# Kernel tuning notes

Measured on AMD Instinct MI355X. Metric: run time of the kernel, lower is better.

Reference implementation:

```python
import jax, jax.numpy as jnp
import numpy as np

D_IN, N_HEADS, N_KV, HEAD_DIM = 2048, 8, 4, 256
GROUP = N_HEADS // N_KV
SCALING = 256.0 ** -0.5  # query_pre_attn_scalar = 256
EPS = 1e-6


def _rms_norm(x, gamma):
    # Gemma-style RMSNorm with (1 + gamma) scale, over last dim (head_dim)
    var = jnp.mean(x * x, axis=-1, keepdims=True)
    return x * jax.lax.rsqrt(var + EPS) * (1.0 + gamma)


def _apply_rope(x, cos, sin):
    # x: [b, h, s, d]; cos/sin: [s, d] (rotate-half convention)
    d = x.shape[-1]
    x1, x2 = x[..., : d // 2], x[..., d // 2:]
    rotated = jnp.concatenate([-x2, x1], axis=-1)
    return x * cos[None, None] + rotated * sin[None, None]


def setup_inputs() -> dict:
    key = jax.random.key(0)
    ks = jax.random.split(key, 6)
    b, s = 2, 2048
    x = jax.random.normal(ks[0], (b, s, D_IN), dtype=jnp.float32)
    # causal mask: True above diagonal = masked
    mask = jnp.triu(jnp.ones((s, s), dtype=bool), k=1)
    # RoPE tables (base 10000)
    inv_freq = 1.0 / (10000.0 ** (jnp.arange(0, HEAD_DIM, 2, dtype=jnp.float32) / HEAD_DIM))
    angles = jnp.arange(s, dtype=jnp.float32)[:, None] * inv_freq[None, :]  # [s, d/2]
    angles = jnp.concatenate([angles, angles], axis=-1)  # [s, d]
    cos, sin = jnp.cos(angles), jnp.sin(angles)
    std = 0.02
    wq = jax.random.normal(ks[1], (N_HEADS * HEAD_DIM, D_IN), dtype=jnp.float32) * std
    wk = jax.random.normal(ks[2], (N_KV * HEAD_DIM, D_IN), dtype=jnp.float32) * std
    wv = jax.random.normal(ks[3], (N_KV * HEAD_DIM, D_IN), dtype=jnp.float32) * std
    wo = jax.random.normal(ks[4], (D_IN, N_HEADS * HEAD_DIM), dtype=jnp.float32) * std
    q_gamma = jnp.zeros((HEAD_DIM,), dtype=jnp.float32)
    k_gamma = jnp.zeros((HEAD_DIM,), dtype=jnp.float32)
    return {"x": x, "mask": mask, "cos": cos, "sin": sin,
            "wq": wq, "wk": wk, "wv": wv, "wo": wo,
            "q_gamma": q_gamma, "k_gamma": k_gamma}


def reference(x, mask, cos, sin, wq, wk, wv, wo, q_gamma, k_gamma):
    b, s, _ = x.shape
    # projections (torch Linear: y = x @ W.T)
    q = (x @ wq.T).reshape(b, s, N_HEADS, HEAD_DIM).transpose(0, 2, 1, 3)  # [b,H,s,d]
    k = (x @ wk.T).reshape(b, s, N_KV, HEAD_DIM).transpose(0, 2, 1, 3)     # [b,G,s,d]
    v = (x @ wv.T).reshape(b, s, N_KV, HEAD_DIM).transpose(0, 2, 1, 3)     # [b,G,s,d]
    q = _rms_norm(q, q_gamma)
    k = _rms_norm(k, k_gamma)
    q = _apply_rope(q, cos, sin) * SCALING
    k = _apply_rope(k, cos, sin)
    # GQA via broadcast (avoids repeat_interleave): head h = g*GROUP + j (group-major)
    qg = q.reshape(b, N_KV, GROUP, s, HEAD_DIM)
    scores = jnp.einsum('bgjqd,bgkd->bgjqk', qg, k)  # [b,G,group,s,s]
    scores = jnp.where(mask[None, None, None], -jnp.inf, scores)
    weights = jax.nn.softmax(scores, axis=-1)
    ctx = jnp.einsum('bgjqk,bgkd->bgjqd', weights, v)  # [b,G,group,s,d]
    ctx = ctx.reshape(b, N_HEADS, s, HEAD_DIM).transpose(0, 2, 1, 3).reshape(b, s, N_HEADS * HEAD_DIM)
    return ctx @ wo.T
```

## Files before the change

kernel.cpp:

```cpp
#include <hip/hip_runtime.h>
#include <math.h>


typedef __bf16 bf16x8 __attribute__((ext_vector_type(8)));
typedef __bf16 bf16x4 __attribute__((ext_vector_type(4)));
typedef float  f32x4  __attribute__((ext_vector_type(4)));

#define MFMA16(a, b, c) __builtin_amdgcn_mfma_f32_16x16x32_bf16(a, b, c, 0, 0, 0)

__device__ __forceinline__ void async16(const __bf16* g, const __bf16* l) {
  __builtin_amdgcn_global_load_lds(
      (__attribute__((address_space(1))) const void*)g,
      (__attribute__((address_space(3))) void*)l, 16, 0, 0);
}

__global__ __launch_bounds__(256) void cast_f32_bf16(
    const float* __restrict__ src, __bf16* __restrict__ dst) {
  const size_t i = ((size_t)blockIdx.x * 256 + threadIdx.x) * 4;
  f32x4 v = *(const f32x4*)(src + i);
  bf16x4 o;
#pragma unroll
  for (int j = 0; j < 4; j++) o[j] = (__bf16)v[j];
  *(bf16x4*)(dst + i) = o;
}

template <typename OT>
__device__ __forceinline__ void gemm_body(const __bf16* A, const __bf16* B,
                                          OT* C, size_t m0, size_t n0,
                                          size_t ccol0, int ldc) {
  constexpr int K = 2048;
  __shared__ __align__(16) __bf16 As[128 * 32];
  __shared__ __align__(16) __bf16 Bs[128 * 32];
  const int tid = threadIdx.x;
  const int wave = tid >> 6, lane = tid & 63;
  const int lr = lane & 15, lq = lane >> 4;
  const int wm = (wave >> 1) * 64, wn = (wave & 1) * 64;

  f32x4 acc[4][4];
#pragma unroll
  for (int i = 0; i < 4; i++)
#pragma unroll
    for (int j = 0; j < 4; j++)
#pragma unroll
      for (int r = 0; r < 4; r++) acc[i][j][r] = 0.f;

  int srow[2], skof[2];
#pragma unroll
  for (int c = 0; c < 2; c++) {
    const int t = wave * 2 + c;
    const int g = t * 8 + (lane >> 3);
    const int cc = (lane & 7) ^ (g & 7);
    srow[c] = g * 2 + (cc >> 2);
    skof[c] = (cc & 3) * 8;
  }

  for (int k0 = 0; k0 < K; k0 += 32) {
#pragma unroll
    for (int c = 0; c < 2; c++) {
      const int t = wave * 2 + c;
      async16(A + (m0 + srow[c]) * K + k0 + skof[c], As + t * 512);
      async16(B + (n0 + srow[c]) * K + k0 + skof[c], Bs + t * 512);
    }
    __syncthreads();
    bf16x8 af[4], bf[4];
#pragma unroll
    for (int i = 0; i < 4; i++) {
      const int row = wm + i * 16 + lr;
      const int g = row >> 1;
      const int p = ((row & 1) * 4 + lq) ^ (g & 7);
      af[i] = *(const bf16x8*)&As[g * 64 + p * 8];
    }
#pragma unroll
    for (int j = 0; j < 4; j++) {
      const int row = wn + j * 16 + lr;
      const int g = row >> 1;
      const int p = ((row & 1) * 4 + lq) ^ (g & 7);
      bf[j] = *(const bf16x8*)&Bs[g * 64 + p * 8];
    }
#pragma unroll
    for (int i = 0; i < 4; i++)
#pragma unroll
      for (int j = 0; j < 4; j++)
        acc[i][j] = MFMA16(af[i], bf[j], acc[i][j]);
    __syncthreads();
  }

#pragma unroll
  for (int i = 0; i < 4; i++)
#pragma unroll
    for (int j = 0; j < 4; j++)
#pragma unroll
      for (int r = 0; r < 4; r++) {
        const size_t row = m0 + wm + i * 16 + lq * 4 + r;
        const size_t col = ccol0 + wn + j * 16 + lr;
        C[row * (size_t)ldc + col] = (OT)acc[i][j][r];
      }
}

template <typename OT>
__global__ __launch_bounds__(256) void gemm_bt(
    const __bf16* __restrict__ A, const __bf16* __restrict__ B,
    OT* __restrict__ C, const int ldc) {
  gemm_body<OT>(A, B, C, (size_t)blockIdx.y * 128, (size_t)blockIdx.x * 128,
                (size_t)blockIdx.x * 128, ldc);
}

__global__ __launch_bounds__(256) void gemm_qkv(
    const __bf16* __restrict__ A, const __bf16* __restrict__ Bq,
    const __bf16* __restrict__ Bk, const __bf16* __restrict__ Bv,
    __bf16* __restrict__ C) {
  const int bx = blockIdx.x;
  const __bf16* B;
  int nl;
  if (bx < 16) { B = Bq; nl = bx; }
  else if (bx < 24) { B = Bk; nl = bx - 16; }
  else { B = Bv; nl = bx - 24; }
  gemm_body<__bf16>(A, B, C, (size_t)blockIdx.y * 128, (size_t)nl * 128,
                    (size_t)bx * 128, 4096);
}

__global__ __launch_bounds__(256) void rmsrope(
    const __bf16* __restrict__ qkv, const float* __restrict__ cosb,
    const float* __restrict__ sinb, const float* __restrict__ qg,
    const float* __restrict__ kg, __bf16* __restrict__ qrot,
    __bf16* __restrict__ krot) {
  const int wave = threadIdx.x >> 6, lane = threadIdx.x & 63;
  const int rid = blockIdx.x * 4 + wave;
  const int m = rid / 12, seg = rid % 12;
  const int b = m >> 11, pos = m & 2047;
  const bool isq = seg < 8;
  const int col = isq ? seg * 256 : 2048 + (seg - 8) * 256;
  const int d = lane * 4;

  bf16x4 xv = *(const bf16x4*)(qkv + (size_t)m * 4096 + col + d);
  float x[4];
#pragma unroll
  for (int i = 0; i < 4; i++) x[i] = (float)xv[i];
  float ss = x[0] * x[0] + x[1] * x[1] + x[2] * x[2] + x[3] * x[3];
#pragma unroll
  for (int off = 1; off < 64; off <<= 1) ss += __shfl_xor(ss, off);
  const float inv = rsqrtf(ss * (1.f / 256.f) + 1e-6f);

  f32x4 gv = *(const f32x4*)((isq ? qg : kg) + d);
  float xn[4];
#pragma unroll
  for (int i = 0; i < 4; i++) xn[i] = x[i] * inv * (1.f + gv[i]);
  float rot[4];
#pragma unroll
  for (int i = 0; i < 4; i++) {
    const float pn = __shfl_xor(xn[i], 32);
    rot[i] = (lane < 32) ? -pn : pn;
  }
  f32x4 cv = *(const f32x4*)(cosb + (size_t)pos * 256 + d);
  f32x4 sv = *(const f32x4*)(sinb + (size_t)pos * 256 + d);
  const float sc = isq ? 0.0625f : 1.f;
  bf16x4 ov;
#pragma unroll
  for (int i = 0; i < 4; i++)
    ov[i] = (__bf16)((xn[i] * cv[i] + rot[i] * sv[i]) * sc);
  __bf16* dst = isq
      ? qrot + ((size_t)(b * 8 + seg) * 2048 + pos) * 256 + d
      : krot + ((size_t)(b * 4 + (seg - 8)) * 2048 + pos) * 256 + d;
  *(bf16x4*)dst = ov;
}

__global__ __launch_bounds__(256) void vtrans(const __bf16* __restrict__ qkv,
                                              __bf16* __restrict__ vT) {
  __shared__ __bf16 tile[64 * 65];
  const int bkv = blockIdx.z;
  const int d0 = blockIdx.y * 64, p0 = blockIdx.x * 64;
  const int t = threadIdx.x;
  const int b = bkv >> 2, kv = bkv & 3;
#pragma unroll
  for (int i = 0; i < 16; i++) {
    const int f = i * 256 + t;
    const int pl = f >> 6, dl = f & 63;
    tile[pl * 65 + dl] =
        qkv[(size_t)(b * 2048 + p0 + pl) * 4096 + 3072 + kv * 256 + d0 + dl];
  }
  __syncthreads();
#pragma unroll
  for (int i = 0; i < 16; i++) {
    const int f = i * 256 + t;
    const int dl = f >> 6, pl = f & 63;
    vT[((size_t)bkv * 256 + d0 + dl) * 2048 + p0 + pl] = tile[pl * 65 + dl];
  }
}

__global__ __launch_bounds__(256) void flash(
    const __bf16* __restrict__ qrot, const __bf16* __restrict__ krot,
    const __bf16* __restrict__ vT, __bf16* __restrict__ ctx) {
  __shared__ __align__(16) __bf16 Ks[2][64 * 256];
  __shared__ __align__(16) __bf16 Vs[2][256 * 64];
  __shared__ __align__(16) __bf16 Ps[4 * 32 * 64];
  const int tid = threadIdx.x, wave = tid >> 6, lane = tid & 63;
  const int lr = lane & 15, lq = lane >> 4;
  const int Q = blockIdx.x;
  const int h = blockIdx.y, b = blockIdx.z, kv = h >> 1;
  const int q0 = Q * 128 + wave * 32;

  bf16x8 qf[2][8];
  {
    const __bf16* qbb = qrot + (size_t)(b * 8 + h) * 2048 * 256;
#pragma unroll
    for (int qi = 0; qi < 2; qi++)
#pragma unroll
      for (int i = 0; i < 8; i++)
        qf[qi][i] = *(const bf16x8*)(qbb + (size_t)(q0 + qi * 16 + lr) * 256 +
                                     i * 32 + lq * 8);
  }
  f32x4 acc[2][16];
#pragma unroll
  for (int qi = 0; qi < 2; qi++)
#pragma unroll
    for (int j = 0; j < 16; j++)
#pragma unroll
      for (int r = 0; r < 4; r++) acc[qi][j][r] = 0.f;
  float lsum[2][4];
#pragma unroll
  for (int qi = 0; qi < 2; qi++)
#pragma unroll
    for (int r = 0; r < 4; r++) lsum[qi][r] = 0.f;

  const __bf16* kbase = krot + (size_t)(b * 4 + kv) * 2048 * 256;
  const __bf16* vbase = vT + (size_t)(b * 4 + kv) * 256 * 2048;

  int koff[8], voff[8];
#pragma unroll
  for (int c = 0; c < 8; c++) {
    const int t = wave * 8 + c;
    {
      const int row = t * 2 + (lane >> 5);
      const int ch = (lane & 31) ^ (row & 31);
      koff[c] = row * 256 + ch * 8;
    }
    {
      const int d = t * 8 + (lane >> 3);
      const int ch = (lane & 7) ^ (d & 7);
      voff[c] = d * 2048 + ch * 8;
    }
  }

  const int nt = 2 * Q + 2;

#define STAGE(kt_, buf_)                                                   \
  {                                                                        \
    const int k0_ = (kt_)*64;                                              \
    _Pragma("unroll") for (int c = 0; c < 8; c++) {                        \
      const int t = wave * 8 + c;                                          \
      async16(kbase + (size_t)k0_ * 256 + koff[c], Ks[buf_] + t * 512);    \
      async16(vbase + k0_ + voff[c], Vs[buf_] + t * 512);                  \
    }                                                                      \
  }

  STAGE(0, 0);

  for (int kt = 0; kt < nt; kt++) {
    const int cur = kt & 1;
    const int k0 = kt * 64;
    if (kt + 1 < nt) {
      STAGE(kt + 1, cur ^ 1);
      asm volatile("s_waitcnt vmcnt(16)" ::: "memory");
    } else {
      asm volatile("s_waitcnt vmcnt(0)" ::: "memory");
    }
    __builtin_amdgcn_s_barrier();

    f32x4 s[2][4];
#pragma unroll
    for (int qi = 0; qi < 2; qi++)
#pragma unroll
      for (int f = 0; f < 4; f++)
#pragma unroll
        for (int r = 0; r < 4; r++) s[qi][f][r] = 0.f;
#pragma unroll
    for (int i = 0; i < 8; i++) {
      bf16x8 kf[4];
#pragma unroll
      for (int f = 0; f < 4; f++) {
        const int row = f * 16 + lr;
        const int pch = (i * 4 + lq) ^ (row & 31);
        kf[f] = *(const bf16x8*)&Ks[cur][row * 256 + pch * 8];
      }
#pragma unroll
      for (int qi = 0; qi < 2; qi++)
#pragma unroll
        for (int f = 0; f < 4; f++)
          s[qi][f] = MFMA16(qf[qi][i], kf[f], s[qi][f]);
    }

    const bool diag = (k0 + 63 > q0);
#pragma unroll
    for (int qi = 0; qi < 2; qi++) {
      const int qa = q0 + qi * 16 + lq * 4;
#pragma unroll
      for (int f = 0; f < 4; f++) {
        const int ka = k0 + f * 16 + lr;
        const int row = qi * 16 + lq * 4;
        const int pchb = (f * 2 + (lr >> 3));
#pragma unroll
        for (int r = 0; r < 4; r++) {
          float p = __expf(s[qi][f][r] - 16.f);
          if (diag && ka > qa + r) p = 0.f;
          lsum[qi][r] += p;
          Ps[wave * 2048 + (row + r) * 64 + (pchb ^ ((row + r) & 7)) * 8 +
             (lr & 7)] = (__bf16)p;
        }
      }
    }
    asm volatile("s_waitcnt lgkmcnt(0)" ::: "memory");

#pragma unroll
    for (int m = 0; m < 2; m++) {
      bf16x8 pf[2];
#pragma unroll
      for (int qi = 0; qi < 2; qi++) {
        const int row = qi * 16 + lr;
        const int pch = (m * 4 + lq) ^ (row & 7);
        pf[qi] = *(const bf16x8*)&Ps[wave * 2048 + row * 64 + pch * 8];
      }
#pragma unroll
      for (int j = 0; j < 16; j++) {
        const int d = j * 16 + lr;
        const int pch = (m * 4 + lq) ^ (d & 7);
        bf16x8 vf = *(const bf16x8*)&Vs[cur][d * 64 + pch * 8];
#pragma unroll
        for (int qi = 0; qi < 2; qi++)
          acc[qi][j] = MFMA16(pf[qi], vf, acc[qi][j]);
      }
    }
    __builtin_amdgcn_s_barrier();
  }
#undef STAGE

  float inv[2][4];
#pragma unroll
  for (int qi = 0; qi < 2; qi++)
#pragma unroll
    for (int r = 0; r < 4; r++) {
      float l = lsum[qi][r];
#pragma unroll
      for (int off = 1; off < 16; off <<= 1) l += __shfl_xor(l, off);
      inv[qi][r] = 1.f / l;
    }
#pragma unroll
  for (int qi = 0; qi < 2; qi++)
#pragma unroll
    for (int j = 0; j < 16; j++)
#pragma unroll
      for (int r = 0; r < 4; r++) {
        const int row = q0 + qi * 16 + lq * 4 + r;
        ctx[((size_t)(b * 2048 + row) * 8 + h) * 256 + j * 16 + lr] =
            (__bf16)(acc[qi][j][r] * inv[qi][r]);
      }
}

extern "C" void kernel_launch(void* const* d_in, const int* in_sizes, int n_in,
                              void* d_out, int out_size, void* d_ws,
                              size_t ws_size, hipStream_t stream) {
  const float* x = (const float*)d_in[0];
  const float* cosb = (const float*)d_in[2];
  const float* sinb = (const float*)d_in[3];
  const float* wq = (const float*)d_in[4];
  const float* wk = (const float*)d_in[5];
  const float* wv = (const float*)d_in[6];
  const float* wo = (const float*)d_in[7];
  const float* qg = (const float*)d_in[8];
  const float* kg = (const float*)d_in[9];
  float* out = (float*)d_out;

  char* ws = (char*)d_ws;
  __bf16* xbf = (__bf16*)ws;
  __bf16* wqbf = (__bf16*)(ws + ((size_t)16 << 20));
  __bf16* wkbf = (__bf16*)(ws + ((size_t)24 << 20));
  __bf16* wvbf = (__bf16*)(ws + ((size_t)28 << 20));
  __bf16* qkv = (__bf16*)(ws + ((size_t)32 << 20));
  __bf16* qrot = (__bf16*)ws;
  __bf16* krot = (__bf16*)(ws + ((size_t)16 << 20));
  __bf16* vTp = (__bf16*)(ws + ((size_t)24 << 20));
  __bf16* wobf = (__bf16*)(ws + ((size_t)32 << 20));
  __bf16* ctx = (__bf16*)(ws + ((size_t)40 << 20));

  cast_f32_bf16<<<8192, 256, 0, stream>>>(x, xbf);
  cast_f32_bf16<<<4096, 256, 0, stream>>>(wq, wqbf);
  cast_f32_bf16<<<2048, 256, 0, stream>>>(wk, wkbf);
  cast_f32_bf16<<<2048, 256, 0, stream>>>(wv, wvbf);

  gemm_qkv<<<dim3(32, 32), 256, 0, stream>>>(xbf, wqbf, wkbf, wvbf, qkv);

  rmsrope<<<12288, 256, 0, stream>>>(qkv, cosb, sinb, qg, kg, qrot, krot);
  vtrans<<<dim3(32, 4, 8), 256, 0, stream>>>(qkv, vTp);

  cast_f32_bf16<<<4096, 256, 0, stream>>>(wo, wobf);
  flash<<<dim3(16, 8, 2), 256, 0, stream>>>(qrot, krot, vTp, ctx);

  gemm_bt<float><<<dim3(16, 32), 256, 0, stream>>>(ctx, wobf, out, 2048);
}
```

Baseline: 425.8 us.

## Stage K/V tiles through registers instead of async global-to-LDS loads

```diff
diff --git a/kernel.cpp b/kernel.cpp
--- a/kernel.cpp
+++ b/kernel.cpp
@@ -187,7 +187,7 @@
   }
 }
 
-__global__ __launch_bounds__(256) void flash(
+__global__ __launch_bounds__(256, 1) void flash(
     const __bf16* __restrict__ qrot, const __bf16* __restrict__ krot,
     const __bf16* __restrict__ vT, __bf16* __restrict__ ctx) {
   __shared__ __align__(16) __bf16 Ks[2][64 * 256];
@@ -243,28 +243,33 @@
 
   const int nt = 2 * Q + 2;
 
-#define STAGE(kt_, buf_)                                                   \
+  bf16x8 kreg[8], vreg[8];
+
+#define KVLOAD(kt_)                                                        \
   {                                                                        \
     const int k0_ = (kt_)*64;                                              \
     _Pragma("unroll") for (int c = 0; c < 8; c++) {                        \
+      kreg[c] = *(const bf16x8*)(kbase + (size_t)k0_ * 256 + koff[c]);     \
+      vreg[c] = *(const bf16x8*)(vbase + k0_ + voff[c]);                   \
+    }                                                                      \
+  }
+#define KVWRITE(buf_)                                                      \
+  {                                                                        \
+    _Pragma("unroll") for (int c = 0; c < 8; c++) {                        \
       const int t = wave * 8 + c;                                          \
-      async16(kbase + (size_t)k0_ * 256 + koff[c], Ks[buf_] + t * 512);    \
-      async16(vbase + k0_ + voff[c], Vs[buf_] + t * 512);                  \
+      *(bf16x8*)&Ks[buf_][t * 512 + lane * 8] = kreg[c];                   \
+      *(bf16x8*)&Vs[buf_][t * 512 + lane * 8] = vreg[c];                   \
     }                                                                      \
   }
 
-  STAGE(0, 0);
+  KVLOAD(0);
+  KVWRITE(0);
+  __syncthreads();
 
   for (int kt = 0; kt < nt; kt++) {
     const int cur = kt & 1;
     const int k0 = kt * 64;
-    if (kt + 1 < nt) {
-      STAGE(kt + 1, cur ^ 1);
-      asm volatile("s_waitcnt vmcnt(16)" ::: "memory");
-    } else {
-      asm volatile("s_waitcnt vmcnt(0)" ::: "memory");
-    }
-    __builtin_amdgcn_s_barrier();
+    if (kt + 1 < nt) KVLOAD(kt + 1);
 
     f32x4 s[2][4];
 #pragma unroll
@@ -329,9 +334,12 @@
           acc[qi][j] = MFMA16(pf[qi], vf, acc[qi][j]);
       }
     }
-    __builtin_amdgcn_s_barrier();
-  }
-#undef STAGE
+
+    if (kt + 1 < nt) KVWRITE(cur ^ 1);
+    __syncthreads();
+  }
+#undef KVLOAD
+#undef KVWRITE
 
   float inv[2][4];
 #pragma unroll
```

Measured after the change: 434.2 us. No clear change (+2.0%).
